# Optimization experiments

Hardware: AMD Instinct MI355X
Metric: run time of the kernel (lower is better)

## Reference

```python
import jax, jax.numpy as jnp
import numpy as np

N_NODES = 50000
N_EDGES = 1_600_000
IN_DIM = 256
OUT_DIM = 128
NEG_SLOPE = 0.01  # F.leaky_relu default


def setup_inputs() -> dict:
    key = jax.random.key(0)
    k1, k2, k3, k4, k5 = jax.random.split(key, 5)
    x = jax.random.normal(k1, (N_NODES, IN_DIM), dtype=jnp.float32)
    # glorot_init: uniform in [-r, r], r = sqrt(6/(in+out))
    r = np.sqrt(6.0 / (IN_DIM + OUT_DIM)).astype(np.float32)
    weight = jax.random.uniform(k2, (IN_DIM, OUT_DIM), dtype=jnp.float32, minval=-r, maxval=r)
    adj_rows = jax.random.randint(k3, (N_EDGES,), 0, N_NODES, dtype=jnp.int64 if jax.config.jax_enable_x64 else jnp.int32)
    adj_cols = jax.random.randint(k4, (N_EDGES,), 0, N_NODES, dtype=jnp.int64 if jax.config.jax_enable_x64 else jnp.int32)
    adj_vals = jax.random.uniform(k5, (N_EDGES,), dtype=jnp.float32)
    return {"x": x, "weight": weight, "adj_vals": adj_vals,
            "adj_rows": adj_rows, "adj_cols": adj_cols}


def reference(x, weight, adj_vals, adj_rows, adj_cols):
    # h = X @ W : [N, OUT_DIM]
    h = x @ weight
    # sparse adj @ h via edge-list SpMM: out[r] += v * h[c]
    msgs = adj_vals[:, None] * h[adj_cols]            # [E, OUT_DIM]
    agg = jax.ops.segment_sum(msgs, adj_rows, num_segments=N_NODES)
    # leaky_relu epilogue
    return jnp.where(agg >= 0, agg, NEG_SLOPE * agg)
```

## Files before the change

kernel.cpp:

```cpp
#include <hip/hip_runtime.h>
#include <hip/hip_fp16.h>

#define N_NODES 50000
#define N_EDGES 1600000
#define IN_DIM 256
#define OUT_DIM 128
#define NEG_SLOPE 0.01f

#define RB    32
#define NBUCK ((N_NODES + RB - 1) / RB)
#define CAP   1536

#define HIST_BLOCKS 256
#define CONVW_BLOCKS 16
#define EPB_H (N_EDGES / HIST_BLOCKS)
#define SCAT_BLOCKS 512
#define EPB_S (N_EDGES / SCAT_BLOCKS)
#define SCAT_ITERS ((EPB_S + 255) / 256)

typedef _Float16 f16x8 __attribute__((ext_vector_type(8)));
typedef float    f32x4 __attribute__((ext_vector_type(4)));

#define BM 128
#define GEMM_BLOCKS ((N_NODES + BM - 1) / BM)

#define CVT16(lo, hi) do { \
    lo[0]=(_Float16)xr[0].x; lo[1]=(_Float16)xr[0].y; lo[2]=(_Float16)xr[0].z; lo[3]=(_Float16)xr[0].w; \
    lo[4]=(_Float16)xr[1].x; lo[5]=(_Float16)xr[1].y; lo[6]=(_Float16)xr[1].z; lo[7]=(_Float16)xr[1].w; \
    hi[0]=(_Float16)xr[2].x; hi[1]=(_Float16)xr[2].y; hi[2]=(_Float16)xr[2].z; hi[3]=(_Float16)xr[2].w; \
    hi[4]=(_Float16)xr[3].x; hi[5]=(_Float16)xr[3].y; hi[6]=(_Float16)xr[3].z; hi[7]=(_Float16)xr[3].w; \
} while (0)

__global__ __launch_bounds__(256, 2) void gemm_xw_mfma(const float* __restrict__ x,
                                                       const __half* __restrict__ wtl,
                                                       __half* __restrict__ h) {
    __shared__ f16x8 wt8[32 * 128];
    __shared__ f16x8 xs8[2][4][BM];

    const int t    = threadIdx.x;
    const int lane = t & 63;
    const int wv   = t >> 6;
    const int row0 = blockIdx.x * BM;

    {
        const int4* src = (const int4*)wtl;
        int4* dst = (int4*)wt8;
#pragma unroll
        for (int i = 0; i < 16; ++i) dst[i * 256 + t] = src[i * 256 + t];
    }

    const int srow = t >> 1;
    const int skh  = t & 1;
    const int grow = row0 + srow;
    const bool rv  = grow < N_NODES;
    const float* xp = x + (size_t)(rv ? grow : 0) * IN_DIM + skh * 16;

    float4 xr[4];
#pragma unroll
    for (int i = 0; i < 4; ++i)
        xr[i] = rv ? ((const float4*)xp)[i] : make_float4(0.f, 0.f, 0.f, 0.f);
    {
        f16x8 lo, hi;
        CVT16(lo, hi);
        xs8[0][skh * 2 + 0][srow] = lo;
        xs8[0][skh * 2 + 1][srow] = hi;
    }
    __syncthreads();

    f32x4 acc[2][8];
#pragma unroll
    for (int mf = 0; mf < 2; ++mf)
#pragma unroll
        for (int nf = 0; nf < 8; ++nf) acc[mf][nf] = (f32x4){0.f, 0.f, 0.f, 0.f};

    const int kg  = lane >> 4;
    const int l15 = lane & 15;
    const int mb  = (wv << 5) + l15;

#pragma unroll
    for (int ks = 0; ks < 8; ++ks) {
        const int cur = ks & 1;
        if (ks < 7) {
#pragma unroll
            for (int i = 0; i < 4; ++i)
                xr[i] = rv ? ((const float4*)(xp + (ks + 1) * 32))[i]
                           : make_float4(0.f, 0.f, 0.f, 0.f);
        }
        const f16x8 b0 = xs8[cur][kg][mb];
        const f16x8 b1 = xs8[cur][kg][mb + 16];
#pragma unroll
        for (int nf = 0; nf < 8; ++nf) {
            const f16x8 a = wt8[(((ks << 2) | kg) << 7) + (nf << 4) + l15];
            acc[0][nf] = __builtin_amdgcn_mfma_f32_16x16x32_f16(a, b0, acc[0][nf], 0, 0, 0);
            acc[1][nf] = __builtin_amdgcn_mfma_f32_16x16x32_f16(a, b1, acc[1][nf], 0, 0, 0);
        }
        if (ks < 7) {
            f16x8 lo, hi;
            CVT16(lo, hi);
            xs8[cur ^ 1][skh * 2 + 0][srow] = lo;
            xs8[cur ^ 1][skh * 2 + 1][srow] = hi;
            __syncthreads();
        }
    }

    const int rg = lane >> 4;
#pragma unroll
    for (int mf = 0; mf < 2; ++mf) {
        const int m = row0 + (wv << 5) + (mf << 4) + l15;
        if (m < N_NODES) {
            __half* hp = h + (size_t)m * OUT_DIM + (rg << 2);
#pragma unroll
            for (int nf = 0; nf < 8; ++nf) {
                union { ushort4 u; __half f[4]; } o;
                o.f[0] = __float2half(acc[mf][nf][0]);
                o.f[1] = __float2half(acc[mf][nf][1]);
                o.f[2] = __float2half(acc[mf][nf][2]);
                o.f[3] = __float2half(acc[mf][nf][3]);
                *(ushort4*)(hp + (nf << 4)) = o.u;
            }
        }
    }
}

__global__ __launch_bounds__(256) void bucket_hist(const int* __restrict__ rows,
                                                   int* __restrict__ counts,
                                                   const float* __restrict__ w,
                                                   __half* __restrict__ wtl) {
    if (blockIdx.x >= HIST_BLOCKS) {
        const int e0 = ((blockIdx.x - HIST_BLOCKS) * 256 + threadIdx.x) * 8;
        const int k  = e0 >> 7;
        const int n0 = e0 & 127;
        const float4 a = *(const float4*)(w + e0);
        const float4 b = *(const float4*)(w + e0 + 4);
        __half* dst = wtl + ((size_t)((k >> 3) * 128 + n0)) * 8 + (k & 7);
        dst[0]  = __float2half(a.x);
        dst[8]  = __float2half(a.y);
        dst[16] = __float2half(a.z);
        dst[24] = __float2half(a.w);
        dst[32] = __float2half(b.x);
        dst[40] = __float2half(b.y);
        dst[48] = __float2half(b.z);
        dst[56] = __float2half(b.w);
        return;
    }

    __shared__ int lhist[NBUCK];
    const int t = threadIdx.x;
    const int ebase = blockIdx.x * EPB_H;

    for (int b = t; b < NBUCK; b += 256) lhist[b] = 0;
    __syncthreads();

    for (int k = 0; k < EPB_H; k += 256) {
        if (k + t < EPB_H) atomicAdd(&lhist[rows[ebase + k + t] / RB], 1);
    }
    __syncthreads();

    for (int b = t; b < NBUCK; b += 256) {
        const int c = lhist[b];
        if (c > 0) atomicAdd(&counts[b], c);
    }
}

__global__ __launch_bounds__(1024) void scan_buckets(const int* __restrict__ counts,
                                                     int* __restrict__ offsets,
                                                     int* __restrict__ cursor) {
    __shared__ int s[1024];
    const int t = threadIdx.x;
    const int i0 = 2 * t, i1 = 2 * t + 1;
    const int v0 = (i0 < NBUCK) ? counts[i0] : 0;
    const int v1 = (i1 < NBUCK) ? counts[i1] : 0;
    s[t] = v0 + v1;
    __syncthreads();
    for (int off = 1; off < 1024; off <<= 1) {
        int u = (t >= off) ? s[t - off] : 0;
        __syncthreads();
        s[t] += u;
        __syncthreads();
    }
    const int excl = s[t] - (v0 + v1);
    if (i0 < NBUCK) { offsets[i0] = excl;      cursor[i0] = excl; }
    if (i1 < NBUCK) { offsets[i1] = excl + v0; cursor[i1] = excl + v0; }
    if (t == 1023) offsets[NBUCK] = s[t];
}

__global__ __launch_bounds__(256) void bucket_scatter(const int* __restrict__ rows,
                                                      const int* __restrict__ cols,
                                                      const float* __restrict__ vals,
                                                      int* __restrict__ cursor,
                                                      int2* __restrict__ ebuf) {
    __shared__ int lcur[NBUCK];
    const int t = threadIdx.x;
    const int ebase = blockIdx.x * EPB_S;

    for (int b = t; b < NBUCK; b += 256) lcur[b] = 0;
    __syncthreads();

    int myr[SCAT_ITERS];
#pragma unroll
    for (int k = 0; k < SCAT_ITERS; ++k) {
        const int i = k * 256 + t;
        myr[k] = -1;
        if (i < EPB_S) {
            const int r = rows[ebase + i];
            myr[k] = r;
            atomicAdd(&lcur[r / RB], 1);
        }
    }
    __syncthreads();

    for (int b = t; b < NBUCK; b += 256) {
        const int c = lcur[b];
        lcur[b] = (c > 0) ? atomicAdd(&cursor[b], c) : 0;
    }
    __syncthreads();

#pragma unroll
    for (int k = 0; k < SCAT_ITERS; ++k) {
        const int i = k * 256 + t;
        if (i < EPB_S) {
            const int e = ebase + i;
            const int r = myr[k];
            const int pos = atomicAdd(&lcur[r / RB], 1);
            ebuf[pos] = make_int2(cols[e] | ((r & (RB - 1)) << 16), __float_as_int(vals[e]));
        }
    }
}

__global__ __launch_bounds__(256) void bucket_gather(const __half* __restrict__ h,
                                                     const int* __restrict__ offsets,
                                                     const int2* __restrict__ ebuf,
                                                     float* __restrict__ out) {
    __shared__ int2 srec[CAP];
    __shared__ int  hist[RB];
    __shared__ int  rowoff[RB + 1];

    const int t    = threadIdx.x;
    const int bkt  = blockIdx.x;
    const int wave = t >> 6;
    const int lane = t & 63;

    const int base = offsets[bkt];
    const int cnt  = offsets[bkt + 1] - base;

    if (t < RB) hist[t] = 0;
    __syncthreads();

    if (cnt <= CAP) {
        const int* ekey = (const int*)ebuf;
        for (int i = t; i < cnt; i += 256) {
            atomicAdd(&hist[(ekey[2 * (base + i)] >> 16) & (RB - 1)], 1);
        }
        __syncthreads();

        if (t < RB) {
            const int v = hist[t];
            int s = v;
#pragma unroll
            for (int off = 1; off < RB; off <<= 1) {
                const int u = __shfl_up(s, off);
                if (t >= off) s += u;
            }
            rowoff[t + 1] = s;
            hist[t] = s - v;
            if (t == 0) rowoff[0] = 0;
        }
        __syncthreads();

        for (int i = t; i < cnt; i += 256) {
            const int2 rec = ebuf[base + i];
            const int pos = atomicAdd(&hist[(rec.x >> 16) & (RB - 1)], 1);
            srec[pos] = rec;
        }
        __syncthreads();

        for (int rr = 0; rr < RB / 4; ++rr) {
            const int row = wave * (RB / 4) + rr;
            const int beg = rowoff[row];
            const int end = rowoff[row + 1];
            float2 acc0 = make_float2(0.f, 0.f);
            float2 acc1 = make_float2(0.f, 0.f);

            int e = beg;
            for (; e + 4 <= end; e += 4) {
                const int2 r0 = srec[e + 0];
                const int2 r1 = srec[e + 1];
                const int2 r2 = srec[e + 2];
                const int2 r3 = srec[e + 3];
                const float2 m0 = __half22float2(((const __half2*)(h + (size_t)(r0.x & 0xFFFF) * OUT_DIM))[lane]);
                const float2 m1 = __half22float2(((const __half2*)(h + (size_t)(r1.x & 0xFFFF) * OUT_DIM))[lane]);
                const float2 m2 = __half22float2(((const __half2*)(h + (size_t)(r2.x & 0xFFFF) * OUT_DIM))[lane]);
                const float2 m3 = __half22float2(((const __half2*)(h + (size_t)(r3.x & 0xFFFF) * OUT_DIM))[lane]);
                const float v0 = __int_as_float(r0.y);
                const float v1 = __int_as_float(r1.y);
                const float v2 = __int_as_float(r2.y);
                const float v3 = __int_as_float(r3.y);
                acc0.x += v0 * m0.x; acc0.y += v0 * m0.y;
                acc1.x += v1 * m1.x; acc1.y += v1 * m1.y;
                acc0.x += v2 * m2.x; acc0.y += v2 * m2.y;
                acc1.x += v3 * m3.x; acc1.y += v3 * m3.y;
            }
            for (; e < end; ++e) {
                const int2 r0 = srec[e];
                const float2 m0 = __half22float2(((const __half2*)(h + (size_t)(r0.x & 0xFFFF) * OUT_DIM))[lane]);
                const float v0 = __int_as_float(r0.y);
                acc0.x += v0 * m0.x; acc0.y += v0 * m0.y;
            }

            float2 acc = make_float2(acc0.x + acc1.x, acc0.y + acc1.y);
            const int grow = bkt * RB + row;
            if (grow < N_NODES) {
                acc.x = acc.x >= 0.f ? acc.x : NEG_SLOPE * acc.x;
                acc.y = acc.y >= 0.f ? acc.y : NEG_SLOPE * acc.y;
                ((float2*)(out + (size_t)grow * OUT_DIM))[lane] = acc;
            }
        }
    } else {
        for (int rr = 0; rr < RB / 4; ++rr) {
            const int row = wave * (RB / 4) + rr;
            float2 acc = make_float2(0.f, 0.f);
            for (int e = 0; e < cnt; ++e) {
                const int2 rec = ebuf[base + e];
                if (((rec.x >> 16) & (RB - 1)) == row) {
                    const float2 m = __half22float2(((const __half2*)(h + (size_t)(rec.x & 0xFFFF) * OUT_DIM))[lane]);
                    const float v = __int_as_float(rec.y);
                    acc.x += v * m.x; acc.y += v * m.y;
                }
            }
            const int grow = bkt * RB + row;
            if (grow < N_NODES) {
                acc.x = acc.x >= 0.f ? acc.x : NEG_SLOPE * acc.x;
                acc.y = acc.y >= 0.f ? acc.y : NEG_SLOPE * acc.y;
                ((float2*)(out + (size_t)grow * OUT_DIM))[lane] = acc;
            }
        }
    }
}

extern "C" void kernel_launch(void* const* d_in, const int* in_sizes, int n_in,
                              void* d_out, int out_size, void* d_ws, size_t ws_size,
                              hipStream_t stream) {
    const float* x    = (const float*)d_in[0];
    const float* w    = (const float*)d_in[1];
    const float* vals = (const float*)d_in[2];
    const int*   rows = (const int*)d_in[3];
    const int*   cols = (const int*)d_in[4];
    float* out = (float*)d_out;

    char* ws = (char*)d_ws;
    size_t off = 0;
    auto alloc = [&](size_t bytes) {
        void* p = ws + off;
        off = (off + bytes + 255) & ~(size_t)255;
        return p;
    };
    __half* h      = (__half*)alloc((size_t)N_NODES * OUT_DIM * sizeof(__half));
    int2*  ebuf    = (int2*) alloc((size_t)N_EDGES * sizeof(int2));
    __half* wtl    = (__half*)alloc((size_t)IN_DIM * OUT_DIM * sizeof(__half));
    int*   counts  = (int*)  alloc((size_t)NBUCK * sizeof(int));
    int*   offsets = (int*)  alloc((size_t)(NBUCK + 1) * sizeof(int));
    int*   cursor  = (int*)  alloc((size_t)NBUCK * sizeof(int));

    hipMemsetAsync(counts, 0, (size_t)NBUCK * sizeof(int), stream);

    bucket_hist<<<HIST_BLOCKS + CONVW_BLOCKS, 256, 0, stream>>>(rows, counts, w, wtl);
    gemm_xw_mfma<<<GEMM_BLOCKS, 256, 0, stream>>>(x, wtl, h);
    scan_buckets<<<1, 1024, 0, stream>>>(counts, offsets, cursor);
    bucket_scatter<<<SCAT_BLOCKS, 256, 0, stream>>>(rows, cols, vals, cursor, ebuf);
    bucket_gather<<<NBUCK, 256, 0, stream>>>(h, offsets, ebuf, out);
}
```

Measured before the change: 236.5 us.

## Restructure SpMM bucketing into coarse bins with separate row-sort and wide gather

```diff
diff --git a/kernel.cpp b/kernel.cpp
--- a/kernel.cpp
+++ b/kernel.cpp
@@ -7,19 +7,29 @@
 #define OUT_DIM 128
 #define NEG_SLOPE 0.01f
 
-#define RB    32
-#define NBUCK ((N_NODES + RB - 1) / RB)
-#define CAP   1536
-
-#define HIST_BLOCKS 256
+#define BIN_SH    7
+#define BIN_ROWS  128
+#define NBIN      ((N_NODES + BIN_ROWS - 1) / BIN_ROWS)
+#define CAPB      4864
+#define ROWOFF_N  (NBIN * BIN_ROWS + 1)
+
+#define GBLK_ROWS 32
+#define NGBLK     ((N_NODES + GBLK_ROWS - 1) / GBLK_ROWS)
+
+#define HIST_BLOCKS 512
 #define CONVW_BLOCKS 16
 #define EPB_H (N_EDGES / HIST_BLOCKS)
 #define SCAT_BLOCKS 512
 #define EPB_S (N_EDGES / SCAT_BLOCKS)
-#define SCAT_ITERS ((EPB_S + 255) / 256)
+#define SCAT_ITERS ((EPB_S + 511) / 512)
 
 typedef _Float16 f16x8 __attribute__((ext_vector_type(8)));
 typedef float    f32x4 __attribute__((ext_vector_type(4)));
+typedef float    f32x8 __attribute__((ext_vector_type(8)));
+
+__device__ __forceinline__ float lrelu(float v) {
+    return v >= 0.f ? v : NEG_SLOPE * v;
+}
 
 #define BM 128
 #define GEMM_BLOCKS ((N_NODES + BM - 1) / BM)
@@ -144,195 +154,242 @@
         return;
     }
 
-    __shared__ int lhist[NBUCK];
+    __shared__ int lhist[NBIN];
     const int t = threadIdx.x;
     const int ebase = blockIdx.x * EPB_H;
 
-    for (int b = t; b < NBUCK; b += 256) lhist[b] = 0;
+    for (int b = t; b < NBIN; b += 256) lhist[b] = 0;
     __syncthreads();
 
     for (int k = 0; k < EPB_H; k += 256) {
-        if (k + t < EPB_H) atomicAdd(&lhist[rows[ebase + k + t] / RB], 1);
-    }
-    __syncthreads();
-
-    for (int b = t; b < NBUCK; b += 256) {
+        if (k + t < EPB_H) atomicAdd(&lhist[rows[ebase + k + t] >> BIN_SH], 1);
+    }
+    __syncthreads();
+
+    for (int b = t; b < NBIN; b += 256) {
         const int c = lhist[b];
         if (c > 0) atomicAdd(&counts[b], c);
     }
 }
 
-__global__ __launch_bounds__(1024) void scan_buckets(const int* __restrict__ counts,
-                                                     int* __restrict__ offsets,
-                                                     int* __restrict__ cursor) {
-    __shared__ int s[1024];
-    const int t = threadIdx.x;
-    const int i0 = 2 * t, i1 = 2 * t + 1;
-    const int v0 = (i0 < NBUCK) ? counts[i0] : 0;
-    const int v1 = (i1 < NBUCK) ? counts[i1] : 0;
-    s[t] = v0 + v1;
-    __syncthreads();
-    for (int off = 1; off < 1024; off <<= 1) {
-        int u = (t >= off) ? s[t - off] : 0;
-        __syncthreads();
-        s[t] += u;
-        __syncthreads();
-    }
-    const int excl = s[t] - (v0 + v1);
-    if (i0 < NBUCK) { offsets[i0] = excl;      cursor[i0] = excl; }
-    if (i1 < NBUCK) { offsets[i1] = excl + v0; cursor[i1] = excl + v0; }
-    if (t == 1023) offsets[NBUCK] = s[t];
-}
-
-__global__ __launch_bounds__(256) void bucket_scatter(const int* __restrict__ rows,
-                                                      const int* __restrict__ cols,
-                                                      const float* __restrict__ vals,
-                                                      int* __restrict__ cursor,
-                                                      int2* __restrict__ ebuf) {
-    __shared__ int lcur[NBUCK];
+__global__ __launch_bounds__(512) void scatter_bins(const int* __restrict__ rows,
+                                                    const int* __restrict__ cols,
+                                                    const float* __restrict__ vals,
+                                                    const int* __restrict__ counts,
+                                                    int* __restrict__ cursor,
+                                                    int2* __restrict__ ebuf) {
+    __shared__ int sb[512];
+    __shared__ int lbase[NBIN];
     const int t = threadIdx.x;
     const int ebase = blockIdx.x * EPB_S;
 
-    for (int b = t; b < NBUCK; b += 256) lcur[b] = 0;
+    sb[t] = (t < NBIN) ? counts[t] : 0;
+    const int myc = sb[t];
+    __syncthreads();
+    for (int off = 1; off < 512; off <<= 1) {
+        const int u = (t >= off) ? sb[t - off] : 0;
+        __syncthreads();
+        sb[t] += u;
+        __syncthreads();
+    }
+    if (t < NBIN) lbase[t] = sb[t] - myc;
+    __syncthreads();
+    if (t < NBIN) sb[t] = 0;
     __syncthreads();
 
     int myr[SCAT_ITERS];
 #pragma unroll
     for (int k = 0; k < SCAT_ITERS; ++k) {
-        const int i = k * 256 + t;
+        const int i = k * 512 + t;
         myr[k] = -1;
         if (i < EPB_S) {
             const int r = rows[ebase + i];
             myr[k] = r;
-            atomicAdd(&lcur[r / RB], 1);
-        }
-    }
-    __syncthreads();
-
-    for (int b = t; b < NBUCK; b += 256) {
-        const int c = lcur[b];
-        lcur[b] = (c > 0) ? atomicAdd(&cursor[b], c) : 0;
+            atomicAdd(&sb[r >> BIN_SH], 1);
+        }
+    }
+    __syncthreads();
+
+    if (t < NBIN) {
+        const int c = sb[t];
+        sb[t] = (c > 0) ? (lbase[t] + atomicAdd(&cursor[t], c)) : 0;
     }
     __syncthreads();
 
 #pragma unroll
     for (int k = 0; k < SCAT_ITERS; ++k) {
-        const int i = k * 256 + t;
+        const int i = k * 512 + t;
         if (i < EPB_S) {
             const int e = ebase + i;
             const int r = myr[k];
-            const int pos = atomicAdd(&lcur[r / RB], 1);
-            ebuf[pos] = make_int2(cols[e] | ((r & (RB - 1)) << 16), __float_as_int(vals[e]));
-        }
-    }
-}
-
-__global__ __launch_bounds__(256) void bucket_gather(const __half* __restrict__ h,
-                                                     const int* __restrict__ offsets,
-                                                     const int2* __restrict__ ebuf,
-                                                     float* __restrict__ out) {
-    __shared__ int2 srec[CAP];
-    __shared__ int  hist[RB];
-    __shared__ int  rowoff[RB + 1];
-
+            const int pos = atomicAdd(&sb[r >> BIN_SH], 1);
+            ebuf[pos] = make_int2(cols[e] | ((r & (BIN_ROWS - 1)) << 16), __float_as_int(vals[e]));
+        }
+    }
+}
+
+__global__ __launch_bounds__(512) void sort_bins(const int* __restrict__ counts,
+                                                 int2* __restrict__ ebuf,
+                                                 int* __restrict__ rowoff,
+                                                 int* __restrict__ ovf) {
+    __shared__ int2 srec[CAPB];
+    __shared__ int sb[512];
+    __shared__ int hist[BIN_ROWS];
+    __shared__ int pfx[BIN_ROWS];
+    __shared__ int s_base, s_cnt;
+
+    const int t   = threadIdx.x;
+    const int bin = blockIdx.x;
+
+    sb[t] = (t < NBIN) ? counts[t] : 0;
+    const int myc = sb[t];
+    __syncthreads();
+    for (int off = 1; off < 512; off <<= 1) {
+        const int u = (t >= off) ? sb[t - off] : 0;
+        __syncthreads();
+        sb[t] += u;
+        __syncthreads();
+    }
+    if (t == bin) { s_base = sb[t] - myc; s_cnt = myc; }
+    if (t < BIN_ROWS) hist[t] = 0;
+    __syncthreads();
+    const int base = s_base;
+    const int cnt  = s_cnt;
+
+    if (cnt <= CAPB) {
+        for (int i = t; i < cnt; i += 512) {
+            const int2 r = ebuf[base + i];
+            srec[i] = r;
+            atomicAdd(&hist[(r.x >> 16) & (BIN_ROWS - 1)], 1);
+        }
+        __syncthreads();
+
+        if (t < BIN_ROWS) pfx[t] = hist[t];
+        __syncthreads();
+        for (int off = 1; off < BIN_ROWS; off <<= 1) {
+            const int u = (t >= off && t < BIN_ROWS) ? pfx[t - off] : 0;
+            __syncthreads();
+            if (t < BIN_ROWS) pfx[t] += u;
+            __syncthreads();
+        }
+        if (t < BIN_ROWS) {
+            const int excl = pfx[t] - hist[t];
+            rowoff[(bin << BIN_SH) + t] = base + excl;
+            if (t == BIN_ROWS - 1) rowoff[(bin << BIN_SH) + BIN_ROWS] = base + cnt;
+            hist[t] = excl;
+        }
+        __syncthreads();
+
+        for (int i = t; i < cnt; i += 512) {
+            const int2 r = srec[i];
+            const int pos = base + atomicAdd(&hist[(r.x >> 16) & (BIN_ROWS - 1)], 1);
+            ebuf[pos] = r;
+        }
+    } else {
+        if (t == 0) ovf[bin] = 1;
+        for (int i = t; i < cnt; i += 512)
+            atomicAdd(&hist[(ebuf[base + i].x >> 16) & (BIN_ROWS - 1)], 1);
+        __syncthreads();
+        if (t < BIN_ROWS) pfx[t] = hist[t];
+        __syncthreads();
+        for (int off = 1; off < BIN_ROWS; off <<= 1) {
+            const int u = (t >= off && t < BIN_ROWS) ? pfx[t - off] : 0;
+            __syncthreads();
+            if (t < BIN_ROWS) pfx[t] += u;
+            __syncthreads();
+        }
+        if (t < BIN_ROWS) {
+            rowoff[(bin << BIN_SH) + t] = base + (pfx[t] - hist[t]);
+            if (t == BIN_ROWS - 1) rowoff[(bin << BIN_SH) + BIN_ROWS] = base + cnt;
+        }
+    }
+}
+
+__global__ __launch_bounds__(256) void gather_rows(const __half* __restrict__ h,
+                                                   const int* __restrict__ rowoff,
+                                                   const int2* __restrict__ ebuf,
+                                                   const int* __restrict__ ovf,
+                                                   float* __restrict__ out) {
     const int t    = threadIdx.x;
+    const int w    = t >> 6;
+    const int lane = t & 63;
+    const int grp  = lane >> 4;
+    const int gl   = lane & 15;
     const int bkt  = blockIdx.x;
-    const int wave = t >> 6;
-    const int lane = t & 63;
-
-    const int base = offsets[bkt];
-    const int cnt  = offsets[bkt + 1] - base;
-
-    if (t < RB) hist[t] = 0;
-    __syncthreads();
-
-    if (cnt <= CAP) {
-        const int* ekey = (const int*)ebuf;
-        for (int i = t; i < cnt; i += 256) {
-            atomicAdd(&hist[(ekey[2 * (base + i)] >> 16) & (RB - 1)], 1);
-        }
-        __syncthreads();
-
-        if (t < RB) {
-            const int v = hist[t];
-            int s = v;
-#pragma unroll
-            for (int off = 1; off < RB; off <<= 1) {
-                const int u = __shfl_up(s, off);
-                if (t >= off) s += u;
-            }
-            rowoff[t + 1] = s;
-            hist[t] = s - v;
-            if (t == 0) rowoff[0] = 0;
-        }
-        __syncthreads();
-
-        for (int i = t; i < cnt; i += 256) {
-            const int2 rec = ebuf[base + i];
-            const int pos = atomicAdd(&hist[(rec.x >> 16) & (RB - 1)], 1);
-            srec[pos] = rec;
-        }
-        __syncthreads();
-
-        for (int rr = 0; rr < RB / 4; ++rr) {
-            const int row = wave * (RB / 4) + rr;
-            const int beg = rowoff[row];
-            const int end = rowoff[row + 1];
-            float2 acc0 = make_float2(0.f, 0.f);
-            float2 acc1 = make_float2(0.f, 0.f);
-
-            int e = beg;
-            for (; e + 4 <= end; e += 4) {
-                const int2 r0 = srec[e + 0];
-                const int2 r1 = srec[e + 1];
-                const int2 r2 = srec[e + 2];
-                const int2 r3 = srec[e + 3];
-                const float2 m0 = __half22float2(((const __half2*)(h + (size_t)(r0.x & 0xFFFF) * OUT_DIM))[lane]);
-                const float2 m1 = __half22float2(((const __half2*)(h + (size_t)(r1.x & 0xFFFF) * OUT_DIM))[lane]);
-                const float2 m2 = __half22float2(((const __half2*)(h + (size_t)(r2.x & 0xFFFF) * OUT_DIM))[lane]);
-                const float2 m3 = __half22float2(((const __half2*)(h + (size_t)(r3.x & 0xFFFF) * OUT_DIM))[lane]);
-                const float v0 = __int_as_float(r0.y);
-                const float v1 = __int_as_float(r1.y);
-                const float v2 = __int_as_float(r2.y);
-                const float v3 = __int_as_float(r3.y);
-                acc0.x += v0 * m0.x; acc0.y += v0 * m0.y;
-                acc1.x += v1 * m1.x; acc1.y += v1 * m1.y;
-                acc0.x += v2 * m2.x; acc0.y += v2 * m2.y;
-                acc1.x += v3 * m3.x; acc1.y += v3 * m3.y;
-            }
-            for (; e < end; ++e) {
-                const int2 r0 = srec[e];
-                const float2 m0 = __half22float2(((const __half2*)(h + (size_t)(r0.x & 0xFFFF) * OUT_DIM))[lane]);
-                const float v0 = __int_as_float(r0.y);
-                acc0.x += v0 * m0.x; acc0.y += v0 * m0.y;
-            }
-
-            float2 acc = make_float2(acc0.x + acc1.x, acc0.y + acc1.y);
-            const int grow = bkt * RB + row;
-            if (grow < N_NODES) {
-                acc.x = acc.x >= 0.f ? acc.x : NEG_SLOPE * acc.x;
-                acc.y = acc.y >= 0.f ? acc.y : NEG_SLOPE * acc.y;
-                ((float2*)(out + (size_t)grow * OUT_DIM))[lane] = acc;
-            }
-        }
-    } else {
-        for (int rr = 0; rr < RB / 4; ++rr) {
-            const int row = wave * (RB / 4) + rr;
+    const int bin  = bkt >> 2;
+    const int rbase = bkt * GBLK_ROWS + w * 8;
+
+    if (ovf[bin]) {
+        const int bb = rowoff[bin << BIN_SH];
+        const int be = rowoff[(bin << BIN_SH) + BIN_ROWS];
+        for (int rr = 0; rr < 8; ++rr) {
+            const int row = rbase + rr;
             float2 acc = make_float2(0.f, 0.f);
-            for (int e = 0; e < cnt; ++e) {
-                const int2 rec = ebuf[base + e];
-                if (((rec.x >> 16) & (RB - 1)) == row) {
+            for (int e = bb; e < be; ++e) {
+                const int2 rec = ebuf[e];
+                if (((rec.x >> 16) & (BIN_ROWS - 1)) == (row & (BIN_ROWS - 1))) {
                     const float2 m = __half22float2(((const __half2*)(h + (size_t)(rec.x & 0xFFFF) * OUT_DIM))[lane]);
                     const float v = __int_as_float(rec.y);
                     acc.x += v * m.x; acc.y += v * m.y;
                 }
             }
-            const int grow = bkt * RB + row;
-            if (grow < N_NODES) {
-                acc.x = acc.x >= 0.f ? acc.x : NEG_SLOPE * acc.x;
-                acc.y = acc.y >= 0.f ? acc.y : NEG_SLOPE * acc.y;
-                ((float2*)(out + (size_t)grow * OUT_DIM))[lane] = acc;
+            if (row < N_NODES) {
+                acc.x = lrelu(acc.x); acc.y = lrelu(acc.y);
+                ((float2*)(out + (size_t)row * OUT_DIM))[lane] = acc;
             }
+        }
+        return;
+    }
+
+    for (int p = 0; p < 4; ++p) {
+        const int r0 = rbase + 2 * p;
+        const int r1 = r0 + 1;
+        const int b0 = rowoff[r0], e0 = rowoff[r0 + 1];
+        const int b1 = rowoff[r1], e1 = rowoff[r1 + 1];
+        const int n0 = e0 - b0, n1 = e1 - b1;
+        const int nmax = n0 > n1 ? n0 : n1;
+        const int iters = (nmax + 3) >> 2;
+
+        f32x8 a0 = (f32x8){0.f,0.f,0.f,0.f,0.f,0.f,0.f,0.f};
+        f32x8 a1 = (f32x8){0.f,0.f,0.f,0.f,0.f,0.f,0.f,0.f};
+
+        for (int it = 0; it < iters; ++it) {
+            const int i0 = b0 + (it << 2) + grp;
+            const int i1 = b1 + (it << 2) + grp;
+            const bool v0i = i0 < e0;
+            const bool v1i = i1 < e1;
+            const int2 rA = ebuf[v0i ? i0 : 0];
+            const int2 rB = ebuf[v1i ? i1 : 0];
+            const float vA = v0i ? __int_as_float(rA.y) : 0.f;
+            const float vB = v1i ? __int_as_float(rB.y) : 0.f;
+            const f16x8 hA = *(const f16x8*)(h + (size_t)(rA.x & 0xFFFF) * OUT_DIM + (gl << 3));
+            const f16x8 hB = *(const f16x8*)(h + (size_t)(rB.x & 0xFFFF) * OUT_DIM + (gl << 3));
+#pragma unroll
+            for (int j = 0; j < 8; ++j) {
+                a0[j] += vA * (float)hA[j];
+                a1[j] += vB * (float)hB[j];
+            }
+        }
+
+#pragma unroll
+        for (int j = 0; j < 8; ++j) {
+            float x0 = a0[j], x1 = a1[j];
+            x0 += __shfl_xor(x0, 16); x0 += __shfl_xor(x0, 32);
+            x1 += __shfl_xor(x1, 16); x1 += __shfl_xor(x1, 32);
+            a0[j] = x0; a1[j] = x1;
+        }
+
+        const int row = (grp & 2) ? r1 : r0;
+        float q[4];
+#pragma unroll
+        for (int k = 0; k < 4; ++k) {
+            const float lo = (grp & 2) ? a1[k]     : a0[k];
+            const float hi = (grp & 2) ? a1[k + 4] : a0[k + 4];
+            q[k] = lrelu((grp & 1) ? hi : lo);
+        }
+        if (row < N_NODES) {
+            float4 o = make_float4(q[0], q[1], q[2], q[3]);
+            *(float4*)(out + (size_t)row * OUT_DIM + (gl << 3) + ((grp & 1) << 2)) = o;
         }
     }
 }
@@ -357,15 +414,17 @@
     __half* h      = (__half*)alloc((size_t)N_NODES * OUT_DIM * sizeof(__half));
     int2*  ebuf    = (int2*) alloc((size_t)N_EDGES * sizeof(int2));
     __half* wtl    = (__half*)alloc((size_t)IN_DIM * OUT_DIM * sizeof(__half));
-    int*   counts  = (int*)  alloc((size_t)NBUCK * sizeof(int));
-    int*   offsets = (int*)  alloc((size_t)(NBUCK + 1) * sizeof(int));
-    int*   cursor  = (int*)  alloc((size_t)NBUCK * sizeof(int));
-
-    hipMemsetAsync(counts, 0, (size_t)NBUCK * sizeof(int), stream);
+    int*   rowoff  = (int*)  alloc((size_t)ROWOFF_N * sizeof(int));
+    int*   meta    = (int*)  alloc((size_t)(3 * NBIN) * sizeof(int));
+    int*   counts  = meta;
+    int*   cursor  = meta + NBIN;
+    int*   ovfl    = meta + 2 * NBIN;
+
+    hipMemsetAsync(meta, 0, (size_t)(3 * NBIN) * sizeof(int), stream);
 
     bucket_hist<<<HIST_BLOCKS + CONVW_BLOCKS, 256, 0, stream>>>(rows, counts, w, wtl);
     gemm_xw_mfma<<<GEMM_BLOCKS, 256, 0, stream>>>(x, wtl, h);
-    scan_buckets<<<1, 1024, 0, stream>>>(counts, offsets, cursor);
-    bucket_scatter<<<SCAT_BLOCKS, 256, 0, stream>>>(rows, cols, vals, cursor, ebuf);
-    bucket_gather<<<NBUCK, 256, 0, stream>>>(h, offsets, ebuf, out);
-}
+    scatter_bins<<<SCAT_BLOCKS, 512, 0, stream>>>(rows, cols, vals, counts, cursor, ebuf);
+    sort_bins<<<NBIN, 512, 0, stream>>>(counts, ebuf, rowoff, ovfl);
+    gather_rows<<<NGBLK, 256, 0, stream>>>(h, rowoff, ebuf, ovfl, out);
+}
```

Measured after the change: 238.6 us. No clear change (+0.9%).
